# Kernel tuning notes

Hardware: AMD Instinct MI355X
Metric: run time of the kernel (lower is better)

Reference implementation:

```python
import jax, jax.numpy as jnp
import numpy as np

B, N, E = 2, 2048, 1024
H = 16
BM = 32  # BLOCK_M
BN = 32  # BLOCK_N
BUDGET = 0.2


def setup_inputs() -> dict:
    key = jax.random.key(0)
    ks = jax.random.split(key, 5)
    w = lambda k: jax.random.normal(k, (E, E), jnp.float32) * 0.02
    return {
        "x": jax.random.normal(ks[0], (B, N, E), jnp.float32),
        "W_Q": w(ks[1]),
        "W_K": w(ks[2]),
        "W_V": w(ks[3]),
        "W_O": w(ks[4]),
    }


def _forward(x, W_Q, W_K, W_V, W_O):
    Bx, Nx, Ex = x.shape
    D = Ex // H
    Tr, Tc = Nx // BM, Nx // BN
    k = max(1, int(BUDGET * Tc))

    def heads(t):  # [B,N,E] -> [B,H,N,D]
        return t.reshape(Bx, Nx, H, D).transpose(0, 2, 1, 3)

    Q = heads(x @ W_Q)
    K = heads(x @ W_K)
    V = heads(x @ W_V)

    # dynamic top-k block routing on mean-pooled blocks (indices are constants)
    Qp = Q.reshape(Bx, H, Tr, BM, D).mean(axis=3)   # [B,H,Tr,D]
    Kp = K.reshape(Bx, H, Tc, BN, D).mean(axis=3)   # [B,H,Tc,D]
    avg_sc = jnp.einsum("bhid,bhjd->bhij", Qp, Kp).mean(axis=(0, 1))  # [Tr,Tc]
    _, idx = jax.lax.top_k(avg_sc, k)  # [Tr,k] selected key blocks per query block

    # gather selected K/V blocks: [B,H,Tr,k,BN,D]
    Kb = K.reshape(Bx, H, Tc, BN, D)
    Vb = V.reshape(Bx, H, Tc, BN, D)
    Ksel = Kb[:, :, idx]
    Vsel = Vb[:, :, idx]

    Qb = Q.reshape(Bx, H, Tr, BM, D)
    scale = 1.0 / jnp.sqrt(jnp.asarray(D, jnp.float32))
    # logits over the union of selected key columns: [B,H,Tr,BM,k*BN]
    logits = jnp.einsum("bhtqd,bhtknd->bhtqkn", Qb, Ksel).reshape(
        Bx, H, Tr, BM, k * BN) * scale
    P = jax.nn.softmax(logits, axis=-1)
    Ob = jnp.einsum("bhtqs,bhtsd->bhtqd", P,
                    Vsel.reshape(Bx, H, Tr, k * BN, D))  # [B,H,Tr,BM,D]
    O = Ob.reshape(Bx, H, Nx, D).transpose(0, 2, 1, 3).reshape(Bx, Nx, Ex)
    return O @ W_O


def reference(x, W_Q, W_K, W_V, W_O):
    return _forward(x, W_Q, W_K, W_V, W_O)
```

## Files before the change

kernel.cpp:

```cpp
#include <hip/hip_runtime.h>
#include <hip/hip_bf16.h>
#include <stdint.h>

#define E     1024
#define NSEQ  2048
#define NH    16
#define HD    64
#define KSEL  12
#define MROWS 4096

typedef unsigned short u16;
typedef __attribute__((ext_vector_type(8))) short bf16x8;
typedef __attribute__((ext_vector_type(4))) float f32x4;
typedef __attribute__((ext_vector_type(4))) unsigned short u16x4;

__device__ __forceinline__ float b2f(u16 u) {
  return __builtin_bit_cast(float, (unsigned)u << 16);
}
__device__ __forceinline__ u16 f2b(float f) {
  return __builtin_bit_cast(u16, __float2bfloat16(f));
}

__device__ __forceinline__ void gload_lds16(const void* g, void* l) {
  auto gp = reinterpret_cast<__attribute__((address_space(1))) unsigned int*>(
      reinterpret_cast<uintptr_t>(g));
  auto lp = reinterpret_cast<__attribute__((address_space(3))) unsigned int*>(
      reinterpret_cast<uintptr_t>(l));
  __builtin_amdgcn_global_load_lds(gp, lp, 16, 0, 0);
}

__global__ void prep_k(const void* __restrict__ xin,
                       const void* __restrict__ w0, const void* __restrict__ w1,
                       const void* __restrict__ w2, const void* __restrict__ w3,
                       u16* __restrict__ xc, u16* __restrict__ Wt,
                       float* __restrict__ xp, int* __restrict__ flagOut) {
  __shared__ u16 tile[64][66];
  __shared__ int flagL;
  const int id = blockIdx.x, tid = threadIdx.x;
  if (tid < 64) {
    const u16* xu = (const u16*)xin;
    int cnt = 0;
    for (int i = tid; i < 1024; i += 64) {
      const unsigned e = (xu[i] >> 7) & 0xFF;
      cnt += (e >= 100 && e <= 140) ? 1 : 0;
    }
#pragma unroll
    for (int off = 1; off < 64; off <<= 1) cnt += __shfl_xor(cnt, off, 64);
    if (tid == 0) flagL = (cnt > 900) ? 1 : 0;
  }
  __syncthreads();
  const int f = flagL;
  if (id == 0 && tid == 0) flagOut[0] = f;

  if (id < 1024) {
    const int n4 = MROWS * E / 4;
    if (f) {
      const u16x4* s = (const u16x4*)xin;
      u16x4* d = (u16x4*)xc;
      for (int i = id * 256 + tid; i < n4; i += 1024 * 256) d[i] = s[i];
    } else {
      const f32x4* s = (const f32x4*)xin;
      for (int i = id * 256 + tid; i < n4; i += 1024 * 256) {
        const f32x4 v = s[i];
        u16x4 o;
        o.x = f2b(v.x); o.y = f2b(v.y); o.z = f2b(v.z); o.w = f2b(v.w);
        *(u16x4*)(xc + (size_t)i * 4) = o;
      }
    }
  } else if (id < 2048) {
    const int tt = id - 1024;
    const int mat = tt >> 8, q = tt & 255;
    const int bn = (q & 15) * 64, bk = (q >> 4) * 64;
    const void* W = mat == 0 ? w0 : mat == 1 ? w1 : mat == 2 ? w2 : w3;
    u16* O = Wt + (size_t)mat * (E * E);
    const int tx = tid & 63, ty = tid >> 6;
    if (f) {
      const u16* Wu = (const u16*)W;
#pragma unroll
      for (int i = 0; i < 16; ++i) {
        const int r = ty + 4 * i;
        tile[r][tx] = Wu[(size_t)(bk + r) * E + bn + tx];
      }
    } else {
      const float* Wf = (const float*)W;
#pragma unroll
      for (int i = 0; i < 16; ++i) {
        const int r = ty + 4 * i;
        tile[r][tx] = f2b(Wf[(size_t)(bk + r) * E + bn + tx]);
      }
    }
    __syncthreads();
#pragma unroll
    for (int i = 0; i < 16; ++i) {
      const int rr = ty + 4 * i;
      O[(size_t)(bn + rr) * E + bk + tx] = tile[tx][rr];
    }
  } else {
    const int blk = id - 2048;
    const size_t base = (size_t)blk * 32 * E;
    if (f) {
      const u16* x = (const u16*)xin;
      for (int c = tid; c < E; c += 256) {
        float s = 0.f;
        for (int r = 0; r < 32; ++r) s += b2f(x[base + (size_t)r * E + c]);
        xp[(size_t)blk * E + c] = s * (1.0f / 32.0f);
      }
    } else {
      const float* x = (const float*)xin;
      for (int c = tid; c < E; c += 256) {
        float s = 0.f;
        for (int r = 0; r < 32; ++r) s += x[base + (size_t)r * E + c];
        xp[(size_t)blk * E + c] = s * (1.0f / 32.0f);
      }
    }
  }
}

__global__ void qpkp2_k(const float* __restrict__ xp, const void* __restrict__ Wq,
                        const void* __restrict__ Wk, float* __restrict__ Ppart,
                        const int* __restrict__ flag) {
  __shared__ float xpT[64][129];
  __shared__ float wS[64][64];
  const int c0 = blockIdx.x * 64, k0 = blockIdx.z * 64;
  const int mat = blockIdx.y;
  const int tid = threadIdx.x;
  const int f = flag[0];
  const void* W = mat ? Wk : Wq;
#pragma unroll
  for (int it = 0; it < 32; ++it) {
    const int i = it * 256 + tid;
    const int row = i >> 6, kk = i & 63;
    xpT[kk][row] = xp[(size_t)row * E + k0 + kk];
  }
  if (f) {
    const u16* Wu = (const u16*)W;
#pragma unroll
    for (int it = 0; it < 16; ++it) {
      const int i = it * 256 + tid;
      const int kk = i >> 6, c = i & 63;
      wS[kk][c] = b2f(Wu[(size_t)(k0 + kk) * E + c0 + c]);
    }
  } else {
    const float* Wf = (const float*)W;
#pragma unroll
    for (int it = 0; it < 16; ++it) {
      const int i = it * 256 + tid;
      const int kk = i >> 6, c = i & 63;
      wS[kk][c] = Wf[(size_t)(k0 + kk) * E + c0 + c];
    }
  }
  __syncthreads();
  const int cq = (tid & 15) * 4;
  const int r0 = (tid >> 4) * 8;
  float acc[8][4] = {};
  for (int kk = 0; kk < 64; ++kk) {
    const f32x4 b = *(const f32x4*)&wS[kk][cq];
    float a[8];
#pragma unroll
    for (int j = 0; j < 8; ++j) a[j] = xpT[kk][r0 + j];
#pragma unroll
    for (int j = 0; j < 8; ++j)
#pragma unroll
      for (int c = 0; c < 4; ++c)
        acc[j][c] += a[j] * b[c];
  }
  float* P = Ppart + (size_t)(mat * 16 + blockIdx.z) * 128 * E;
#pragma unroll
  for (int j = 0; j < 8; ++j)
    *(f32x4*)&P[(size_t)(r0 + j) * E + c0 + cq] = *(const f32x4*)acc[j];
}

__global__ void qpred_k(const float* __restrict__ Ppart, float* __restrict__ Qp,
                        float* __restrict__ Kp) {
  const int fidx = blockIdx.x * 256 + threadIdx.x;
  const int mat = fidx >> 15;
  const int rem = fidx & 32767;
  const float* src = Ppart + (size_t)mat * 16 * 128 * E + (size_t)rem * 4;
  f32x4 s = {};
#pragma unroll
  for (int ks = 0; ks < 16; ++ks)
    s += *(const f32x4*)(src + (size_t)ks * 128 * E);
  float* out = mat ? Kp : Qp;
  *(f32x4*)(out + (size_t)rem * 4) = s;
}

__device__ __forceinline__ void gemm_core(const u16* __restrict__ A,
                                          const u16* __restrict__ Bt,
                                          int bm, int bnG, int wave, int lane,
                                          u16* At, u16* Bs, f32x4 (&acc)[4][4]) {
  const int srow = lane >> 2, scol = (lane & 3) * 8;
  const int q4 = lane >> 4, l16 = lane & 15;
  const int wm = (wave >> 1) * 64, wn = (wave & 1) * 64;
  for (int k0 = 0; k0 < E; k0 += 32) {
#pragma unroll
    for (int r = 0; r < 2; ++r) {
      const int c = r * 4 + wave;
      const int row = c * 16 + srow;
      gload_lds16(A + (size_t)(bm + row) * E + k0 + scol, &At[c * 512 + lane * 8]);
      gload_lds16(Bt + (size_t)(bnG + row) * E + k0 + scol, &Bs[c * 512 + lane * 8]);
    }
    __syncthreads();
    bf16x8 af[4], bfr[4];
#pragma unroll
    for (int mi = 0; mi < 4; ++mi)
      af[mi] = *(const bf16x8*)&At[(wm + mi * 16 + l16) * 32 + q4 * 8];
#pragma unroll
    for (int ni = 0; ni < 4; ++ni)
      bfr[ni] = *(const bf16x8*)&Bs[(wn + ni * 16 + l16) * 32 + q4 * 8];
#pragma unroll
    for (int mi = 0; mi < 4; ++mi)
#pragma unroll
      for (int ni = 0; ni < 4; ++ni)
        acc[mi][ni] = __builtin_amdgcn_mfma_f32_16x16x32_bf16(af[mi], bfr[ni], acc[mi][ni], 0, 0, 0);
    __syncthreads();
  }
}

__launch_bounds__(256, 2)
__global__ void gemmsel_k(const u16* __restrict__ A, const u16* __restrict__ WtAll,
                          u16* __restrict__ Qb, const float* __restrict__ Qp,
                          const float* __restrict__ Kp, float* __restrict__ sc) {
  __shared__ __attribute__((aligned(16))) u16 At[128 * 32];
  __shared__ __attribute__((aligned(16))) u16 Bs[128 * 32];
  __shared__ float qrow[2][E];
  __shared__ float red[4][64];
  const int id = blockIdx.x;
  const int tid = threadIdx.x;
  if (id < 768) {
    const int wave = tid >> 6, lane = tid & 63;
    const int q4 = lane >> 4, l16 = lane & 15;
    const int wm = (wave >> 1) * 64, wn = (wave & 1) * 64;
    const int bm = (id & 31) * 128;
    const int by = id >> 5;
    f32x4 acc[4][4] = {};
    gemm_core(A, WtAll, bm, by * 128, wave, lane, At, Bs, acc);
    const int z = by >> 3;
    const int bnw = (by & 7) * 128;
    u16* O = Qb + (size_t)z * 4194304;
    if (z < 2) {
#pragma unroll
      for (int mi = 0; mi < 4; ++mi) {
        const int rg0 = bm + wm + mi * 16 + q4 * 4;
        const int b = rg0 >> 11, n0 = rg0 & 2047;
#pragma unroll
        for (int ni = 0; ni < 4; ++ni) {
          const int cg = bnw + wn + ni * 16 + l16;
          const int h = cg >> 6, d = cg & 63;
          u16* dst = O + (size_t)(b * NH + h) * NSEQ * HD + d;
#pragma unroll
          for (int r = 0; r < 4; ++r)
            dst[(size_t)(n0 + r) * HD] = f2b(acc[mi][ni][r]);
        }
      }
    } else {
#pragma unroll
      for (int mi = 0; mi < 4; ++mi) {
        const int rg0 = bm + wm + mi * 16 + q4 * 4;
        const int b = rg0 >> 11, n0 = rg0 & 2047;
#pragma unroll
        for (int ni = 0; ni < 4; ++ni) {
          const int cg = bnw + wn + ni * 16 + l16;
          const int h = cg >> 6, d = cg & 63;
          u16x4 v;
          v.x = f2b(acc[mi][ni][0]);
          v.y = f2b(acc[mi][ni][1]);
          v.z = f2b(acc[mi][ni][2]);
          v.w = f2b(acc[mi][ni][3]);
          *(u16x4*)(O + ((size_t)(b * NH + h) * HD + d) * NSEQ + n0) = v;
        }
      }
    }
  } else {
    const int i = id - 768;
    const int j = tid & 63, s = tid >> 6;
    for (int e = tid; e < 2 * E; e += 256)
      qrow[e >> 10][e & 1023] = Qp[(size_t)((e >> 10) * 64 + i) * E + (e & 1023)];
    __syncthreads();
    float acc = 0.f;
    for (int b = 0; b < 2; ++b) {
      const float* kr = Kp + (size_t)(b * 64 + j) * E + s * 256;
      const float* qr = qrow[b] + s * 256;
      for (int e = 0; e < 256; e += 4)
        acc += qr[e] * kr[e] + qr[e + 1] * kr[e + 1] + qr[e + 2] * kr[e + 2] + qr[e + 3] * kr[e + 3];
    }
    red[s][j] = acc;
    __syncthreads();
    if (tid < 64)
      sc[i * 64 + tid] = (red[0][tid] + red[1][tid] + red[2][tid] + red[3][tid]) * (1.0f / 32.0f);
  }
}

__launch_bounds__(256, 4)
__global__ void attn_k(const u16* __restrict__ Q, const u16* __restrict__ K,
                       const u16* __restrict__ Vt, const float* __restrict__ sc,
                       u16* __restrict__ Oat) {
  const int id = blockIdx.x;
  const int xcd = id & 7, g = id >> 3;
  const int t = g & 63;
  const int hb = xcd * 4 + (g >> 6);
  const int h = hb & 15, b = hb >> 4;
  const int tid = threadIdx.x, w = tid >> 6, lane = tid & 63;
  const int q4 = lane >> 4, l16 = lane & 15;
  __shared__ __attribute__((aligned(16))) u16 P[32 * 392];
  __shared__ float redm[4][32];
  __shared__ float reds[4][32];
  __shared__ int selL[KSEL];
  const size_t hbo = (size_t)(b * NH + h) * NSEQ * HD;
  const u16* Qh = Q + hbo;
  const u16* Kh = K + hbo;
  const u16* Vh = Vt + hbo;

  if (w == 0) {
    float v = sc[t * 64 + lane];
#pragma unroll
    for (int j = 0; j < KSEL; ++j) {
      const unsigned bits = __float_as_uint(v);
      const unsigned mono = (bits & 0x80000000u) ? ~bits : (bits | 0x80000000u);
      unsigned long long key = ((unsigned long long)mono << 6) | (unsigned)(63 - lane);
#pragma unroll
      for (int off = 1; off < 64; off <<= 1) {
        const unsigned long long o = __shfl_xor(key, off, 64);
        if (o > key) key = o;
      }
      const int s = 63 - (int)(key & 63ull);
      if (lane == 0) selL[j] = s;
      if (lane == s) v = -3.4e38f;
    }
  }
  __syncthreads();
  int blks[3];
#pragma unroll
  for (int i = 0; i < 3; ++i) blks[i] = selL[w * 3 + i];

  f32x4 accS[2][6] = {};
#pragma unroll
  for (int ks = 0; ks < 2; ++ks) {
    bf16x8 aq[2];
#pragma unroll
    for (int mi = 0; mi < 2; ++mi)
      aq[mi] = *(const bf16x8*)&Qh[(size_t)(t * 32 + mi * 16 + l16) * HD + ks * 32 + q4 * 8];
#pragma unroll
    for (int ni = 0; ni < 6; ++ni) {
      const int n = blks[ni >> 1] * 32 + (ni & 1) * 16 + l16;
      bf16x8 bk = *(const bf16x8*)&Kh[(size_t)n * HD + ks * 32 + q4 * 8];
#pragma unroll
      for (int mi = 0; mi < 2; ++mi)
        accS[mi][ni] = __builtin_amdgcn_mfma_f32_16x16x32_bf16(aq[mi], bk, accS[mi][ni], 0, 0, 0);
    }
  }

  float rmax[2][4];
#pragma unroll
  for (int mi = 0; mi < 2; ++mi)
#pragma unroll
    for (int r = 0; r < 4; ++r) {
      float m = accS[mi][0][r];
#pragma unroll
      for (int ni = 1; ni < 6; ++ni) m = fmaxf(m, accS[mi][ni][r]);
      rmax[mi][r] = m;
    }
#pragma unroll
  for (int off = 1; off < 16; off <<= 1)
#pragma unroll
    for (int mi = 0; mi < 2; ++mi)
#pragma unroll
      for (int r = 0; r < 4; ++r)
        rmax[mi][r] = fmaxf(rmax[mi][r], __shfl_xor(rmax[mi][r], off, 64));
  if (l16 == 0) {
#pragma unroll
    for (int mi = 0; mi < 2; ++mi)
#pragma unroll
      for (int r = 0; r < 4; ++r)
        redm[w][mi * 16 + q4 * 4 + r] = rmax[mi][r];
  }
  __syncthreads();
  const float cexp = 0.125f * 1.44269504088896f;
  float gmax[2][4];
#pragma unroll
  for (int mi = 0; mi < 2; ++mi)
#pragma unroll
    for (int r = 0; r < 4; ++r) {
      const int row = mi * 16 + q4 * 4 + r;
      gmax[mi][r] = fmaxf(fmaxf(redm[0][row], redm[1][row]), fmaxf(redm[2][row], redm[3][row]));
    }
  float rsum[2][4] = {};
#pragma unroll
  for (int mi = 0; mi < 2; ++mi)
#pragma unroll
    for (int ni = 0; ni < 6; ++ni)
#pragma unroll
      for (int r = 0; r < 4; ++r) {
        const float e = __builtin_exp2f((accS[mi][ni][r] - gmax[mi][r]) * cexp);
        accS[mi][ni][r] = e;
        rsum[mi][r] += e;
      }
#pragma unroll
  for (int off = 1; off < 16; off <<= 1)
#pragma unroll
    for (int mi = 0; mi < 2; ++mi)
#pragma unroll
      for (int r = 0; r < 4; ++r)
        rsum[mi][r] += __shfl_xor(rsum[mi][r], off, 64);
  if (l16 == 0) {
#pragma unroll
    for (int mi = 0; mi < 2; ++mi)
#pragma unroll
      for (int r = 0; r < 4; ++r)
        reds[w][mi * 16 + q4 * 4 + r] = rsum[mi][r];
  }
  __syncthreads();
#pragma unroll
  for (int mi = 0; mi < 2; ++mi)
#pragma unroll
    for (int r = 0; r < 4; ++r) {
      const int row = mi * 16 + q4 * 4 + r;
      const float inv = 1.0f / (reds[0][row] + reds[1][row] + reds[2][row] + reds[3][row]);
#pragma unroll
      for (int ni = 0; ni < 6; ++ni)
        P[row * 392 + w * 96 + ni * 16 + l16] = f2b(accS[mi][ni][r] * inv);
    }
  __syncthreads();

  f32x4 accO[2] = {};
#pragma unroll
  for (int q = 0; q < KSEL; ++q) {
    const int blk = selL[q];
    const bf16x8 bv = *(const bf16x8*)&Vh[(size_t)(w * 16 + l16) * NSEQ + blk * 32 + q4 * 8];
#pragma unroll
    for (int mi = 0; mi < 2; ++mi) {
      const bf16x8 ap = *(const bf16x8*)&P[(mi * 16 + l16) * 392 + q * 32 + q4 * 8];
      accO[mi] = __builtin_amdgcn_mfma_f32_16x16x32_bf16(ap, bv, accO[mi], 0, 0, 0);
    }
  }
#pragma unroll
  for (int mi = 0; mi < 2; ++mi) {
    const int row0 = t * 32 + mi * 16 + q4 * 4;
#pragma unroll
    for (int r = 0; r < 4; ++r)
      Oat[(size_t)(b * NSEQ + row0 + r) * E + h * HD + w * 16 + l16] = f2b(accO[mi][r]);
  }
}

__launch_bounds__(256, 2)
__global__ void gemmo_k(const u16* __restrict__ A, const u16* __restrict__ Wot,
                        void* __restrict__ OutBase, const int* __restrict__ flag) {
  __shared__ __attribute__((aligned(16))) u16 At[128 * 32];
  __shared__ __attribute__((aligned(16))) u16 Bs[128 * 32];
  const int tid = threadIdx.x;
  const int wave = tid >> 6, lane = tid & 63;
  const int q4 = lane >> 4, l16 = lane & 15;
  const int wm = (wave >> 1) * 64, wn = (wave & 1) * 64;
  const int bm = blockIdx.x * 128, bn = blockIdx.y * 128;
  f32x4 acc[4][4] = {};
  gemm_core(A, Wot, bm, bn, wave, lane, At, Bs, acc);
  const int f = flag[0];
  if (f) {
    u16* Out = (u16*)OutBase;
#pragma unroll
    for (int mi = 0; mi < 4; ++mi) {
      const int rg0 = bm + wm + mi * 16 + q4 * 4;
#pragma unroll
      for (int ni = 0; ni < 4; ++ni) {
        const int cg = bn + wn + ni * 16 + l16;
#pragma unroll
        for (int r = 0; r < 4; ++r)
          Out[(size_t)(rg0 + r) * E + cg] = f2b(acc[mi][ni][r]);
      }
    }
  } else {
    float* Out = (float*)OutBase;
#pragma unroll
    for (int mi = 0; mi < 4; ++mi) {
      const int rg0 = bm + wm + mi * 16 + q4 * 4;
#pragma unroll
      for (int ni = 0; ni < 4; ++ni) {
        const int cg = bn + wn + ni * 16 + l16;
#pragma unroll
        for (int r = 0; r < 4; ++r)
          Out[(size_t)(rg0 + r) * E + cg] = acc[mi][ni][r];
      }
    }
  }
}

extern "C" void kernel_launch(void* const* d_in, const int* in_sizes, int n_in,
                              void* d_out, int out_size, void* d_ws, size_t ws_size,
                              hipStream_t stream) {
  (void)in_sizes; (void)n_in; (void)out_size; (void)ws_size;
  const void* x  = d_in[0];
  const void* wq = d_in[1];
  const void* wk = d_in[2];
  const void* wv = d_in[3];
  const void* wo = d_in[4];

  u16* Wt  = (u16*)d_ws;
  u16* Qb  = Wt + 4 * 1048576;
  u16* Oat = Qb + 3 * 4194304;
  u16* xc  = Oat;
  float* Ppart = (float*)Qb;
  float* xp = (float*)(Oat + 4194304);
  float* Qp = xp + 131072;
  float* Kp = Qp + 131072;
  float* sc = Kp + 131072;
  int* flag = (int*)(sc + 4096) + 768;

  prep_k<<<dim3(2176), 256, 0, stream>>>(x, wq, wk, wv, wo, xc, Wt, xp, flag);
  qpkp2_k<<<dim3(16, 2, 16), 256, 0, stream>>>(xp, wq, wk, Ppart, flag);
  qpred_k<<<dim3(256), 256, 0, stream>>>(Ppart, Qp, Kp);
  gemmsel_k<<<dim3(832), 256, 0, stream>>>(xc, Wt, Qb, Qp, Kp, sc);
  attn_k<<<dim3(2048), 256, 0, stream>>>(Qb, Qb + 4194304, Qb + 2 * 4194304, sc, Oat);
  gemmo_k<<<dim3(32, 8), 256, 0, stream>>>(Oat, Wt + 3 * 1048576, d_out, flag);
}
```

Baseline: 206.8 us.

## Replace split-K pooled projection with direct kernel and remap GEMM tiles per XCD

The split-K pooled Q/K projection and its separate reduction kernel become one kernel in which each thread computes two output columns over the full K dimension. This removes a launch and the partial-sum buffer round trip, but gives up shared-memory reuse and each thread now runs a long serial K loop. The QKV and output GEMMs now map block IDs to tiles so that each XCD handles a contiguous group of M rows, aiming for better L2 reuse. The score path reuses the GEMM's shared-memory buffers to cut LDS use.

```diff
diff --git a/kernel.cpp b/kernel.cpp
--- a/kernel.cpp
+++ b/kernel.cpp
@@ -11,6 +11,7 @@
 
 typedef unsigned short u16;
 typedef __attribute__((ext_vector_type(8))) short bf16x8;
+typedef __attribute__((ext_vector_type(2))) float f32x2;
 typedef __attribute__((ext_vector_type(4))) float f32x4;
 typedef __attribute__((ext_vector_type(4))) unsigned short u16x4;
 
@@ -116,72 +117,39 @@
   }
 }
 
-__global__ void qpkp2_k(const float* __restrict__ xp, const void* __restrict__ Wq,
-                        const void* __restrict__ Wk, float* __restrict__ Ppart,
-                        const int* __restrict__ flag) {
-  __shared__ float xpT[64][129];
-  __shared__ float wS[64][64];
-  const int c0 = blockIdx.x * 64, k0 = blockIdx.z * 64;
-  const int mat = blockIdx.y;
-  const int tid = threadIdx.x;
+__global__ void qpkp3_k(const float* __restrict__ xp, const void* __restrict__ Wq,
+                        const void* __restrict__ Wk, float* __restrict__ Qp,
+                        float* __restrict__ Kp, const int* __restrict__ flag) {
+  const int sid = blockIdx.x, tid = threadIdx.x;
+  const int mat = sid >> 8, q = sid & 255;
+  const int c0 = (q & 15) * 64, r0 = (q >> 4) * 8;
   const int f = flag[0];
+  const int row = r0 + (tid >> 5);
+  const int col = c0 + (tid & 31) * 2;
   const void* W = mat ? Wk : Wq;
-#pragma unroll
-  for (int it = 0; it < 32; ++it) {
-    const int i = it * 256 + tid;
-    const int row = i >> 6, kk = i & 63;
-    xpT[kk][row] = xp[(size_t)row * E + k0 + kk];
-  }
+  const float* xr = xp + (size_t)row * E;
+  float a0 = 0.f, a1 = 0.f;
   if (f) {
-    const u16* Wu = (const u16*)W;
-#pragma unroll
-    for (int it = 0; it < 16; ++it) {
-      const int i = it * 256 + tid;
-      const int kk = i >> 6, c = i & 63;
-      wS[kk][c] = b2f(Wu[(size_t)(k0 + kk) * E + c0 + c]);
+    const u16* Wu = (const u16*)W + col;
+#pragma unroll 4
+    for (int k = 0; k < E; ++k) {
+      const float xv = xr[k];
+      a0 += xv * b2f(Wu[(size_t)k * E]);
+      a1 += xv * b2f(Wu[(size_t)k * E + 1]);
     }
   } else {
-    const float* Wf = (const float*)W;
-#pragma unroll
-    for (int it = 0; it < 16; ++it) {
-      const int i = it * 256 + tid;
-      const int kk = i >> 6, c = i & 63;
-      wS[kk][c] = Wf[(size_t)(k0 + kk) * E + c0 + c];
-    }
-  }
-  __syncthreads();
-  const int cq = (tid & 15) * 4;
-  const int r0 = (tid >> 4) * 8;
-  float acc[8][4] = {};
-  for (int kk = 0; kk < 64; ++kk) {
-    const f32x4 b = *(const f32x4*)&wS[kk][cq];
-    float a[8];
-#pragma unroll
-    for (int j = 0; j < 8; ++j) a[j] = xpT[kk][r0 + j];
-#pragma unroll
-    for (int j = 0; j < 8; ++j)
-#pragma unroll
-      for (int c = 0; c < 4; ++c)
-        acc[j][c] += a[j] * b[c];
-  }
-  float* P = Ppart + (size_t)(mat * 16 + blockIdx.z) * 128 * E;
-#pragma unroll
-  for (int j = 0; j < 8; ++j)
-    *(f32x4*)&P[(size_t)(r0 + j) * E + c0 + cq] = *(const f32x4*)acc[j];
-}
-
-__global__ void qpred_k(const float* __restrict__ Ppart, float* __restrict__ Qp,
-                        float* __restrict__ Kp) {
-  const int fidx = blockIdx.x * 256 + threadIdx.x;
-  const int mat = fidx >> 15;
-  const int rem = fidx & 32767;
-  const float* src = Ppart + (size_t)mat * 16 * 128 * E + (size_t)rem * 4;
-  f32x4 s = {};
-#pragma unroll
-  for (int ks = 0; ks < 16; ++ks)
-    s += *(const f32x4*)(src + (size_t)ks * 128 * E);
-  float* out = mat ? Kp : Qp;
-  *(f32x4*)(out + (size_t)rem * 4) = s;
+    const float* Wf = (const float*)W + col;
+#pragma unroll 4
+    for (int k = 0; k < E; ++k) {
+      const float xv = xr[k];
+      const f32x2 w = *(const f32x2*)(Wf + (size_t)k * E);
+      a0 += xv * w.x;
+      a1 += xv * w.y;
+    }
+  }
+  float* out = (mat ? Kp : Qp) + (size_t)row * E + col;
+  out[0] = a0;
+  out[1] = a1;
 }
 
 __device__ __forceinline__ void gemm_core(const u16* __restrict__ A,
@@ -216,70 +184,80 @@
   }
 }
 
+__device__ __forceinline__ void qkv_epilogue(f32x4 (&acc)[4][4], u16* __restrict__ Qb,
+                                             int bm, int by, int wave, int lane) {
+  const int q4 = lane >> 4, l16 = lane & 15;
+  const int wm = (wave >> 1) * 64, wn = (wave & 1) * 64;
+  const int z = by >> 3;
+  const int bnw = (by & 7) * 128;
+  u16* O = Qb + (size_t)z * 4194304;
+  if (z < 2) {
+#pragma unroll
+    for (int mi = 0; mi < 4; ++mi) {
+      const int rg0 = bm + wm + mi * 16 + q4 * 4;
+      const int b = rg0 >> 11, n0 = rg0 & 2047;
+#pragma unroll
+      for (int ni = 0; ni < 4; ++ni) {
+        const int cg = bnw + wn + ni * 16 + l16;
+        const int h = cg >> 6, d = cg & 63;
+        u16* dst = O + (size_t)(b * NH + h) * NSEQ * HD + d;
+#pragma unroll
+        for (int r = 0; r < 4; ++r)
+          dst[(size_t)(n0 + r) * HD] = f2b(acc[mi][ni][r]);
+      }
+    }
+  } else {
+#pragma unroll
+    for (int mi = 0; mi < 4; ++mi) {
+      const int rg0 = bm + wm + mi * 16 + q4 * 4;
+      const int b = rg0 >> 11, n0 = rg0 & 2047;
+#pragma unroll
+      for (int ni = 0; ni < 4; ++ni) {
+        const int cg = bnw + wn + ni * 16 + l16;
+        const int h = cg >> 6, d = cg & 63;
+        u16x4 v;
+        v.x = f2b(acc[mi][ni][0]);
+        v.y = f2b(acc[mi][ni][1]);
+        v.z = f2b(acc[mi][ni][2]);
+        v.w = f2b(acc[mi][ni][3]);
+        *(u16x4*)(O + ((size_t)(b * NH + h) * HD + d) * NSEQ + n0) = v;
+      }
+    }
+  }
+}
+
 __launch_bounds__(256, 2)
 __global__ void gemmsel_k(const u16* __restrict__ A, const u16* __restrict__ WtAll,
                           u16* __restrict__ Qb, const float* __restrict__ Qp,
                           const float* __restrict__ Kp, float* __restrict__ sc) {
   __shared__ __attribute__((aligned(16))) u16 At[128 * 32];
   __shared__ __attribute__((aligned(16))) u16 Bs[128 * 32];
-  __shared__ float qrow[2][E];
   __shared__ float red[4][64];
   const int id = blockIdx.x;
   const int tid = threadIdx.x;
   if (id < 768) {
     const int wave = tid >> 6, lane = tid & 63;
-    const int q4 = lane >> 4, l16 = lane & 15;
-    const int wm = (wave >> 1) * 64, wn = (wave & 1) * 64;
-    const int bm = (id & 31) * 128;
-    const int by = id >> 5;
+    const int xcd = id & 7, j = id >> 3;
+    const int jm = j / 24;
+    const int mt = (xcd << 2) + jm;
+    const int nt = j - jm * 24;
     f32x4 acc[4][4] = {};
-    gemm_core(A, WtAll, bm, by * 128, wave, lane, At, Bs, acc);
-    const int z = by >> 3;
-    const int bnw = (by & 7) * 128;
-    u16* O = Qb + (size_t)z * 4194304;
-    if (z < 2) {
-#pragma unroll
-      for (int mi = 0; mi < 4; ++mi) {
-        const int rg0 = bm + wm + mi * 16 + q4 * 4;
-        const int b = rg0 >> 11, n0 = rg0 & 2047;
-#pragma unroll
-        for (int ni = 0; ni < 4; ++ni) {
-          const int cg = bnw + wn + ni * 16 + l16;
-          const int h = cg >> 6, d = cg & 63;
-          u16* dst = O + (size_t)(b * NH + h) * NSEQ * HD + d;
-#pragma unroll
-          for (int r = 0; r < 4; ++r)
-            dst[(size_t)(n0 + r) * HD] = f2b(acc[mi][ni][r]);
-        }
-      }
-    } else {
-#pragma unroll
-      for (int mi = 0; mi < 4; ++mi) {
-        const int rg0 = bm + wm + mi * 16 + q4 * 4;
-        const int b = rg0 >> 11, n0 = rg0 & 2047;
-#pragma unroll
-        for (int ni = 0; ni < 4; ++ni) {
-          const int cg = bnw + wn + ni * 16 + l16;
-          const int h = cg >> 6, d = cg & 63;
-          u16x4 v;
-          v.x = f2b(acc[mi][ni][0]);
-          v.y = f2b(acc[mi][ni][1]);
-          v.z = f2b(acc[mi][ni][2]);
-          v.w = f2b(acc[mi][ni][3]);
-          *(u16x4*)(O + ((size_t)(b * NH + h) * HD + d) * NSEQ + n0) = v;
-        }
-      }
-    }
+    gemm_core(A, WtAll, mt * 128, nt * 128, wave, lane, At, Bs, acc);
+    qkv_epilogue(acc, Qb, mt * 128, nt, wave, lane);
   } else {
+    float* qrow0 = (float*)At;
+    float* qrow1 = (float*)Bs;
     const int i = id - 768;
     const int j = tid & 63, s = tid >> 6;
-    for (int e = tid; e < 2 * E; e += 256)
-      qrow[e >> 10][e & 1023] = Qp[(size_t)((e >> 10) * 64 + i) * E + (e & 1023)];
+    for (int e = tid; e < 2 * E; e += 256) {
+      float* dst = (e >> 10) ? qrow1 : qrow0;
+      dst[e & 1023] = Qp[(size_t)((e >> 10) * 64 + i) * E + (e & 1023)];
+    }
     __syncthreads();
     float acc = 0.f;
     for (int b = 0; b < 2; ++b) {
       const float* kr = Kp + (size_t)(b * 64 + j) * E + s * 256;
-      const float* qr = qrow[b] + s * 256;
+      const float* qr = (b ? qrow1 : qrow0) + s * 256;
       for (int e = 0; e < 256; e += 4)
         acc += qr[e] * kr[e] + qr[e + 1] * kr[e + 1] + qr[e + 2] * kr[e + 2] + qr[e + 3] * kr[e + 3];
     }
@@ -450,7 +428,11 @@
   const int wave = tid >> 6, lane = tid & 63;
   const int q4 = lane >> 4, l16 = lane & 15;
   const int wm = (wave >> 1) * 64, wn = (wave & 1) * 64;
-  const int bm = blockIdx.x * 128, bn = blockIdx.y * 128;
+  const int id = blockIdx.x;
+  const int xcd = id & 7, j = id >> 3;
+  const int mt = (xcd << 2) + (j >> 3);
+  const int nt = j & 7;
+  const int bm = mt * 128, bn = nt * 128;
   f32x4 acc[4][4] = {};
   gemm_core(A, Wot, bm, bn, wave, lane, At, Bs, acc);
   const int f = flag[0];
@@ -497,7 +479,6 @@
   u16* Qb  = Wt + 4 * 1048576;
   u16* Oat = Qb + 3 * 4194304;
   u16* xc  = Oat;
-  float* Ppart = (float*)Qb;
   float* xp = (float*)(Oat + 4194304);
   float* Qp = xp + 131072;
   float* Kp = Qp + 131072;
@@ -505,9 +486,8 @@
   int* flag = (int*)(sc + 4096) + 768;
 
   prep_k<<<dim3(2176), 256, 0, stream>>>(x, wq, wk, wv, wo, xc, Wt, xp, flag);
-  qpkp2_k<<<dim3(16, 2, 16), 256, 0, stream>>>(xp, wq, wk, Ppart, flag);
-  qpred_k<<<dim3(256), 256, 0, stream>>>(Ppart, Qp, Kp);
+  qpkp3_k<<<dim3(512), 256, 0, stream>>>(xp, wq, wk, Qp, Kp, flag);
   gemmsel_k<<<dim3(832), 256, 0, stream>>>(xc, Wt, Qb, Qp, Kp, sc);
   attn_k<<<dim3(2048), 256, 0, stream>>>(Qb, Qb + 4194304, Qb + 2 * 4194304, sc, Oat);
-  gemmo_k<<<dim3(32, 8), 256, 0, stream>>>(Oat, Wt + 3 * 1048576, d_out, flag);
-}
+  gemmo_k<<<dim3(256), 256, 0, stream>>>(Oat, Wt + 3 * 1048576, d_out, flag);
+}
```

After: 282.2 us. 1.36x slower.

## Fuse block mean-pooling into conversion and replace split-K reduction with atomics

Applied to the files above, without the earlier changes.

The mean-pooled x rows are now accumulated with float atomics inside the bf16 conversion blocks, so the separate pooling blocks no longer re-read x. The split-K partial buffer and its reduction kernel are replaced by atomic adds straight into Qp/Kp, which removes one launch and a large partial write and read. A memset is added to zero the accumulators, and the selection branch reuses GEMM shared memory instead of its own array to cut LDS use. The risks are atomic contention, an extra memset launch, and nondeterministic summation order that can change top-k ties.

```diff
diff --git a/kernel.cpp b/kernel.cpp
--- a/kernel.cpp
+++ b/kernel.cpp
@@ -53,21 +53,36 @@
   if (id == 0 && tid == 0) flagOut[0] = f;
 
   if (id < 1024) {
-    const int n4 = MROWS * E / 4;
+    f32x4 csum = {};
     if (f) {
       const u16x4* s = (const u16x4*)xin;
       u16x4* d = (u16x4*)xc;
-      for (int i = id * 256 + tid; i < n4; i += 1024 * 256) d[i] = s[i];
+#pragma unroll
+      for (int i = 0; i < 4; ++i) {
+        const int c = id * 1024 + i * 256 + tid;
+        const u16x4 v = s[c];
+        d[c] = v;
+        csum.x += b2f(v.x); csum.y += b2f(v.y);
+        csum.z += b2f(v.z); csum.w += b2f(v.w);
+      }
     } else {
       const f32x4* s = (const f32x4*)xin;
-      for (int i = id * 256 + tid; i < n4; i += 1024 * 256) {
-        const f32x4 v = s[i];
+#pragma unroll
+      for (int i = 0; i < 4; ++i) {
+        const int c = id * 1024 + i * 256 + tid;
+        const f32x4 v = s[c];
         u16x4 o;
         o.x = f2b(v.x); o.y = f2b(v.y); o.z = f2b(v.z); o.w = f2b(v.w);
-        *(u16x4*)(xc + (size_t)i * 4) = o;
-      }
-    }
-  } else if (id < 2048) {
+        *(u16x4*)(xc + (size_t)c * 4) = o;
+        csum += v;
+      }
+    }
+    float* xpt = xp + (size_t)(id >> 3) * E + tid * 4;
+    unsafeAtomicAdd(xpt + 0, csum.x * (1.0f / 32.0f));
+    unsafeAtomicAdd(xpt + 1, csum.y * (1.0f / 32.0f));
+    unsafeAtomicAdd(xpt + 2, csum.z * (1.0f / 32.0f));
+    unsafeAtomicAdd(xpt + 3, csum.w * (1.0f / 32.0f));
+  } else {
     const int tt = id - 1024;
     const int mat = tt >> 8, q = tt & 255;
     const int bn = (q & 15) * 64, bk = (q >> 4) * 64;
@@ -95,30 +110,12 @@
       const int rr = ty + 4 * i;
       O[(size_t)(bn + rr) * E + bk + tx] = tile[tx][rr];
     }
-  } else {
-    const int blk = id - 2048;
-    const size_t base = (size_t)blk * 32 * E;
-    if (f) {
-      const u16* x = (const u16*)xin;
-      for (int c = tid; c < E; c += 256) {
-        float s = 0.f;
-        for (int r = 0; r < 32; ++r) s += b2f(x[base + (size_t)r * E + c]);
-        xp[(size_t)blk * E + c] = s * (1.0f / 32.0f);
-      }
-    } else {
-      const float* x = (const float*)xin;
-      for (int c = tid; c < E; c += 256) {
-        float s = 0.f;
-        for (int r = 0; r < 32; ++r) s += x[base + (size_t)r * E + c];
-        xp[(size_t)blk * E + c] = s * (1.0f / 32.0f);
-      }
-    }
   }
 }
 
 __global__ void qpkp2_k(const float* __restrict__ xp, const void* __restrict__ Wq,
-                        const void* __restrict__ Wk, float* __restrict__ Ppart,
-                        const int* __restrict__ flag) {
+                        const void* __restrict__ Wk, float* __restrict__ Qp,
+                        float* __restrict__ Kp, const int* __restrict__ flag) {
   __shared__ float xpT[64][129];
   __shared__ float wS[64][64];
   const int c0 = blockIdx.x * 64, k0 = blockIdx.z * 64;
@@ -164,24 +161,14 @@
       for (int c = 0; c < 4; ++c)
         acc[j][c] += a[j] * b[c];
   }
-  float* P = Ppart + (size_t)(mat * 16 + blockIdx.z) * 128 * E;
-#pragma unroll
-  for (int j = 0; j < 8; ++j)
-    *(f32x4*)&P[(size_t)(r0 + j) * E + c0 + cq] = *(const f32x4*)acc[j];
-}
-
-__global__ void qpred_k(const float* __restrict__ Ppart, float* __restrict__ Qp,
-                        float* __restrict__ Kp) {
-  const int fidx = blockIdx.x * 256 + threadIdx.x;
-  const int mat = fidx >> 15;
-  const int rem = fidx & 32767;
-  const float* src = Ppart + (size_t)mat * 16 * 128 * E + (size_t)rem * 4;
-  f32x4 s = {};
-#pragma unroll
-  for (int ks = 0; ks < 16; ++ks)
-    s += *(const f32x4*)(src + (size_t)ks * 128 * E);
-  float* out = mat ? Kp : Qp;
-  *(f32x4*)(out + (size_t)rem * 4) = s;
+  float* out = (mat ? Kp : Qp);
+#pragma unroll
+  for (int j = 0; j < 8; ++j) {
+    float* dst = out + (size_t)(r0 + j) * E + c0 + cq;
+#pragma unroll
+    for (int c = 0; c < 4; ++c)
+      unsafeAtomicAdd(dst + c, acc[j][c]);
+  }
 }
 
 __device__ __forceinline__ void gemm_core(const u16* __restrict__ A,
@@ -216,70 +203,78 @@
   }
 }
 
+__device__ __forceinline__ void qkv_epilogue(f32x4 (&acc)[4][4], u16* __restrict__ Qb,
+                                             int bm, int by, int wave, int lane) {
+  const int q4 = lane >> 4, l16 = lane & 15;
+  const int wm = (wave >> 1) * 64, wn = (wave & 1) * 64;
+  const int z = by >> 3;
+  const int bnw = (by & 7) * 128;
+  u16* O = Qb + (size_t)z * 4194304;
+  if (z < 2) {
+#pragma unroll
+    for (int mi = 0; mi < 4; ++mi) {
+      const int rg0 = bm + wm + mi * 16 + q4 * 4;
+      const int b = rg0 >> 11, n0 = rg0 & 2047;
+#pragma unroll
+      for (int ni = 0; ni < 4; ++ni) {
+        const int cg = bnw + wn + ni * 16 + l16;
+        const int h = cg >> 6, d = cg & 63;
+        u16* dst = O + (size_t)(b * NH + h) * NSEQ * HD + d;
+#pragma unroll
+        for (int r = 0; r < 4; ++r)
+          dst[(size_t)(n0 + r) * HD] = f2b(acc[mi][ni][r]);
+      }
+    }
+  } else {
+#pragma unroll
+    for (int mi = 0; mi < 4; ++mi) {
+      const int rg0 = bm + wm + mi * 16 + q4 * 4;
+      const int b = rg0 >> 11, n0 = rg0 & 2047;
+#pragma unroll
+      for (int ni = 0; ni < 4; ++ni) {
+        const int cg = bnw + wn + ni * 16 + l16;
+        const int h = cg >> 6, d = cg & 63;
+        u16x4 v;
+        v.x = f2b(acc[mi][ni][0]);
+        v.y = f2b(acc[mi][ni][1]);
+        v.z = f2b(acc[mi][ni][2]);
+        v.w = f2b(acc[mi][ni][3]);
+        *(u16x4*)(O + ((size_t)(b * NH + h) * HD + d) * NSEQ + n0) = v;
+      }
+    }
+  }
+}
+
 __launch_bounds__(256, 2)
 __global__ void gemmsel_k(const u16* __restrict__ A, const u16* __restrict__ WtAll,
                           u16* __restrict__ Qb, const float* __restrict__ Qp,
                           const float* __restrict__ Kp, float* __restrict__ sc) {
   __shared__ __attribute__((aligned(16))) u16 At[128 * 32];
   __shared__ __attribute__((aligned(16))) u16 Bs[128 * 32];
-  __shared__ float qrow[2][E];
   __shared__ float red[4][64];
   const int id = blockIdx.x;
   const int tid = threadIdx.x;
   if (id < 768) {
     const int wave = tid >> 6, lane = tid & 63;
-    const int q4 = lane >> 4, l16 = lane & 15;
-    const int wm = (wave >> 1) * 64, wn = (wave & 1) * 64;
     const int bm = (id & 31) * 128;
     const int by = id >> 5;
     f32x4 acc[4][4] = {};
     gemm_core(A, WtAll, bm, by * 128, wave, lane, At, Bs, acc);
-    const int z = by >> 3;
-    const int bnw = (by & 7) * 128;
-    u16* O = Qb + (size_t)z * 4194304;
-    if (z < 2) {
-#pragma unroll
-      for (int mi = 0; mi < 4; ++mi) {
-        const int rg0 = bm + wm + mi * 16 + q4 * 4;
-        const int b = rg0 >> 11, n0 = rg0 & 2047;
-#pragma unroll
-        for (int ni = 0; ni < 4; ++ni) {
-          const int cg = bnw + wn + ni * 16 + l16;
-          const int h = cg >> 6, d = cg & 63;
-          u16* dst = O + (size_t)(b * NH + h) * NSEQ * HD + d;
-#pragma unroll
-          for (int r = 0; r < 4; ++r)
-            dst[(size_t)(n0 + r) * HD] = f2b(acc[mi][ni][r]);
-        }
-      }
-    } else {
-#pragma unroll
-      for (int mi = 0; mi < 4; ++mi) {
-        const int rg0 = bm + wm + mi * 16 + q4 * 4;
-        const int b = rg0 >> 11, n0 = rg0 & 2047;
-#pragma unroll
-        for (int ni = 0; ni < 4; ++ni) {
-          const int cg = bnw + wn + ni * 16 + l16;
-          const int h = cg >> 6, d = cg & 63;
-          u16x4 v;
-          v.x = f2b(acc[mi][ni][0]);
-          v.y = f2b(acc[mi][ni][1]);
-          v.z = f2b(acc[mi][ni][2]);
-          v.w = f2b(acc[mi][ni][3]);
-          *(u16x4*)(O + ((size_t)(b * NH + h) * HD + d) * NSEQ + n0) = v;
-        }
-      }
-    }
+    qkv_epilogue(acc, Qb, bm, by, wave, lane);
   } else {
+    float* qrow0 = (float*)At;
+    float* qrow1 = (float*)Bs;
     const int i = id - 768;
     const int j = tid & 63, s = tid >> 6;
-    for (int e = tid; e < 2 * E; e += 256)
-      qrow[e >> 10][e & 1023] = Qp[(size_t)((e >> 10) * 64 + i) * E + (e & 1023)];
+    for (int e = tid; e < 2 * E; e += 256) {
+      float* dst = (e >> 10) ? qrow1 : qrow0;
+      dst[e & 1023] = Qp[(size_t)((e >> 10) * 64 + i) * E + (e & 1023)];
+    }
     __syncthreads();
     float acc = 0.f;
     for (int b = 0; b < 2; ++b) {
       const float* kr = Kp + (size_t)(b * 64 + j) * E + s * 256;
-      const float* qr = qrow[b] + s * 256;
+      const float* qr = (b ? qrow1 : qrow0) + s * 256;
       for (int e = 0; e < 256; e += 4)
         acc += qr[e] * kr[e] + qr[e + 1] * kr[e + 1] + qr[e + 2] * kr[e + 2] + qr[e + 3] * kr[e + 3];
     }
@@ -497,16 +492,15 @@
   u16* Qb  = Wt + 4 * 1048576;
   u16* Oat = Qb + 3 * 4194304;
   u16* xc  = Oat;
-  float* Ppart = (float*)Qb;
   float* xp = (float*)(Oat + 4194304);
   float* Qp = xp + 131072;
   float* Kp = Qp + 131072;
   float* sc = Kp + 131072;
-  int* flag = (int*)(sc + 4096) + 768;
-
-  prep_k<<<dim3(2176), 256, 0, stream>>>(x, wq, wk, wv, wo, xc, Wt, xp, flag);
-  qpkp2_k<<<dim3(16, 2, 16), 256, 0, stream>>>(xp, wq, wk, Ppart, flag);
-  qpred_k<<<dim3(256), 256, 0, stream>>>(Ppart, Qp, Kp);
+  int* flag = (int*)(sc + 4096);
+
+  hipMemsetAsync(xp, 0, 3 * 131072 * sizeof(float), stream);
+  prep_k<<<dim3(2048), 256, 0, stream>>>(x, wq, wk, wv, wo, xc, Wt, xp, flag);
+  qpkp2_k<<<dim3(16, 2, 16), 256, 0, stream>>>(xp, wq, wk, Qp, Kp, flag);
   gemmsel_k<<<dim3(832), 256, 0, stream>>>(xc, Wt, Qb, Qp, Kp, sc);
   attn_k<<<dim3(2048), 256, 0, stream>>>(Qb, Qb + 4194304, Qb + 2 * 4194304, sc, Oat);
   gemmo_k<<<dim3(32, 8), 256, 0, stream>>>(Oat, Wt + 3 * 1048576, d_out, flag);
```

Measured after the change: 262.7 us. +27.0%, slower.
